# Performance work log

Measured on AMD Instinct MI355X. Metric: run time of the kernel, lower is better.

## Reference

```python
import jax, jax.numpy as jnp
import numpy as np

B = 32768
IN_DIM = 768
HIDDENS = [2048, 1024, 512]
EMBED_DIM = 128
NUM_EMB = 1024
DEPTH = 3


def setup_inputs() -> dict:
    key = jax.random.key(0)
    ks = jax.random.split(key, 20)
    d = {"x": jax.random.normal(ks[0], (B, IN_DIM), dtype=jnp.float32)}
    # Encoder: in -> h0 -> h1 -> h2 -> embed  (weights stored as [in, out])
    enc_dims = [IN_DIM] + HIDDENS + [EMBED_DIM]
    for i in range(4):
        fan_in = enc_dims[i]
        d[f"enc_W{i+1}"] = jax.random.normal(ks[1 + i], (enc_dims[i], enc_dims[i + 1]), dtype=jnp.float32) / np.sqrt(fan_in)
        d[f"enc_b{i+1}"] = jnp.zeros((enc_dims[i + 1],), dtype=jnp.float32)
    # Decoder: embed -> h0 -> h1 -> h2 -> in
    dec_dims = [EMBED_DIM] + HIDDENS + [IN_DIM]
    for i in range(4):
        fan_in = dec_dims[i]
        d[f"dec_W{i+1}"] = jax.random.normal(ks[5 + i], (dec_dims[i], dec_dims[i + 1]), dtype=jnp.float32) / np.sqrt(fan_in)
        d[f"dec_b{i+1}"] = jnp.zeros((dec_dims[i + 1],), dtype=jnp.float32)
    # Codebook (nn.Embedding weight, initialized ~ N(0,1) as in the module)
    d["codebook"] = jax.random.normal(ks[9], (NUM_EMB, EMBED_DIM), dtype=jnp.float32)
    return d


def _encoder(x, W1, b1, W2, b2, W3, b3, W4, b4):
    x = jax.nn.relu(x @ W1 + b1)
    x = jax.nn.relu(x @ W2 + b2)
    x = jax.nn.relu(x @ W3 + b3)
    return x @ W4 + b4


def _decoder(x, W1, b1, W2, b2, W3, b3, W4, b4):
    x = jax.nn.relu(x @ W1 + b1)
    x = jax.nn.relu(x @ W2 + b2)
    x = jax.nn.relu(x @ W3 + b3)
    return x @ W4 + b4


def reference(x,
              enc_W1, enc_b1, enc_W2, enc_b2, enc_W3, enc_b3, enc_W4, enc_b4,
              dec_W1, dec_b1, dec_W2, dec_b2, dec_W3, dec_b3, dec_W4, dec_b4,
              codebook):
    z = _encoder(x, enc_W1, enc_b1, enc_W2, enc_b2, enc_W3, enc_b3, enc_W4, enc_b4)
    z_det = jax.lax.stop_gradient(z)

    cb_sq = jnp.sum(codebook * codebook, axis=1)  # [K]
    residue = z_det
    z_hat = jnp.zeros_like(z_det)
    codes = []
    for _ in range(DEPTH):  # residual quantization loop
        # squared L2 distances [B, K]
        dist = (jnp.sum(residue * residue, axis=1, keepdims=True)
                + cb_sq
                - 2.0 * residue @ codebook.T)
        idx = jnp.argmin(dist, axis=1)          # [B]
        codes.append(idx)
        z_hat = z_hat + codebook[idx]           # gather codebook vectors
        residue = z_det - z_hat
    all_codes = jnp.stack(codes, axis=1)        # [B, DEPTH] int

    # straight-through estimator: forward uses z_hat, grad flows through z
    z_flow = z + jax.lax.stop_gradient(z_hat - z)
    x_recon = _decoder(z_flow, dec_W1, dec_b1, dec_W2, dec_b2, dec_W3, dec_b3, dec_W4, dec_b4)
    return (x_recon, all_codes)
```

## Files before the change

kernel.cpp:

```cpp
#include <hip/hip_runtime.h>

#define FLT_MAX_C 3.402823466e+38f

typedef __attribute__((ext_vector_type(8))) __bf16 bf16x8;
typedef __attribute__((ext_vector_type(4))) float f32x4;

static __device__ __forceinline__ ushort f2bf(float x) {
    union { float f; unsigned u; } v; v.f = x;
    unsigned r = (v.u + 0x7FFFu + ((v.u >> 16) & 1u)) >> 16;
    return (ushort)r;
}

template<bool RELU>
__device__ __forceinline__ void gemm_f32_dev(
    const float* __restrict__ A, const float* __restrict__ W,
    const float* __restrict__ bias, float* __restrict__ C, int K, int N)
{
    __shared__ float As[8][128];
    __shared__ float Bs[8][132];
    const int tid = threadIdx.x;
    const int bm = blockIdx.y << 7;
    const int bn = blockIdx.x << 7;

    const int la_row = tid >> 1;
    const int la_k   = (tid & 1) << 2;
    const int lb_row = tid >> 5;
    const int lb_col = (tid & 31) << 2;
    const int tm4 = (tid >> 4) << 2;
    const int tn4 = (tid & 15) << 2;

    float acc[8][8];
    #pragma unroll
    for (int i = 0; i < 8; ++i)
        #pragma unroll
        for (int j = 0; j < 8; ++j) acc[i][j] = 0.f;

    const float* aptr = A + (size_t)(bm + la_row) * K + la_k;
    const float* bptr = W + (size_t)lb_row * N + bn + lb_col;

    float4 av = *(const float4*)(aptr);
    float4 bv = *(const float4*)(bptr);

    for (int k0 = 0; k0 < K; k0 += 8) {
        __syncthreads();
        As[la_k + 0][la_row] = av.x;
        As[la_k + 1][la_row] = av.y;
        As[la_k + 2][la_row] = av.z;
        As[la_k + 3][la_row] = av.w;
        *(float4*)(&Bs[lb_row][lb_col]) = bv;
        __syncthreads();
        if (k0 + 8 < K) {
            av = *(const float4*)(aptr + k0 + 8);
            bv = *(const float4*)(bptr + (size_t)(k0 + 8) * N);
        }
        #pragma unroll
        for (int kk = 0; kk < 8; ++kk) {
            float a[8], b[8];
            *(float4*)(a)     = *(const float4*)(&As[kk][tm4]);
            *(float4*)(a + 4) = *(const float4*)(&As[kk][tm4 + 64]);
            *(float4*)(b)     = *(const float4*)(&Bs[kk][tn4]);
            *(float4*)(b + 4) = *(const float4*)(&Bs[kk][tn4 + 64]);
            #pragma unroll
            for (int i = 0; i < 8; ++i)
                #pragma unroll
                for (int j = 0; j < 8; ++j)
                    acc[i][j] = fmaf(a[i], b[j], acc[i][j]);
        }
    }

    float bv0[8];
    #pragma unroll
    for (int j = 0; j < 8; ++j)
        bv0[j] = bias[bn + tn4 + (j < 4 ? j : 60 + j)];

    #pragma unroll
    for (int i = 0; i < 8; ++i) {
        int row = bm + tm4 + (i < 4 ? i : 60 + i);
        float* cp = C + (size_t)row * N + bn + tn4;
        float4 v0, v1;
        v0.x = acc[i][0] + bv0[0]; v0.y = acc[i][1] + bv0[1];
        v0.z = acc[i][2] + bv0[2]; v0.w = acc[i][3] + bv0[3];
        v1.x = acc[i][4] + bv0[4]; v1.y = acc[i][5] + bv0[5];
        v1.z = acc[i][6] + bv0[6]; v1.w = acc[i][7] + bv0[7];
        if (RELU) {
            v0.x = fmaxf(v0.x, 0.f); v0.y = fmaxf(v0.y, 0.f);
            v0.z = fmaxf(v0.z, 0.f); v0.w = fmaxf(v0.w, 0.f);
            v1.x = fmaxf(v1.x, 0.f); v1.y = fmaxf(v1.y, 0.f);
            v1.z = fmaxf(v1.z, 0.f); v1.w = fmaxf(v1.w, 0.f);
        }
        *(float4*)(cp) = v0;
        *(float4*)(cp + 64) = v1;
    }
}

template<bool RELU>
__device__ __forceinline__ void gemm_f32_wide_dev(
    const float* __restrict__ A, const float* __restrict__ W,
    const float* __restrict__ bias, float* __restrict__ C, int K, int N)
{
    __shared__ float As[8][128];
    __shared__ float Bs[8][260];
    const int tid = threadIdx.x;
    const int bm = blockIdx.y << 7;
    const int bn = blockIdx.x << 8;

    const int la_row = tid >> 1;
    const int la_k   = (tid & 1) << 2;
    const int tm4 = (tid >> 4) << 2;
    const int tn4 = (tid & 15) << 2;
    const int bf_row  = tid >> 6;
    const int bf_col4 = (tid & 63) << 2;

    float acc[8][16];
    #pragma unroll
    for (int i = 0; i < 8; ++i)
        #pragma unroll
        for (int j = 0; j < 16; ++j) acc[i][j] = 0.f;

    const float* aptr = A + (size_t)(bm + la_row) * K + la_k;
    const float* bptr = W + (size_t)bf_row * N + bn + bf_col4;

    float4 av = *(const float4*)(aptr);
    float4 bv0 = *(const float4*)(bptr);
    float4 bv1 = *(const float4*)(bptr + (size_t)4 * N);

    for (int k0 = 0; k0 < K; k0 += 8) {
        __syncthreads();
        As[la_k + 0][la_row] = av.x;
        As[la_k + 1][la_row] = av.y;
        As[la_k + 2][la_row] = av.z;
        As[la_k + 3][la_row] = av.w;
        *(float4*)(&Bs[bf_row][bf_col4])     = bv0;
        *(float4*)(&Bs[bf_row + 4][bf_col4]) = bv1;
        __syncthreads();
        if (k0 + 8 < K) {
            av  = *(const float4*)(aptr + k0 + 8);
            bv0 = *(const float4*)(bptr + (size_t)(k0 + 8) * N);
            bv1 = *(const float4*)(bptr + (size_t)(k0 + 12) * N);
        }
        #pragma unroll
        for (int kk = 0; kk < 8; ++kk) {
            float a[8], b[16];
            *(float4*)(a)      = *(const float4*)(&As[kk][tm4]);
            *(float4*)(a + 4)  = *(const float4*)(&As[kk][tm4 + 64]);
            #pragma unroll
            for (int q = 0; q < 4; ++q)
                *(float4*)(b + q * 4) = *(const float4*)(&Bs[kk][tn4 + 64 * q]);
            #pragma unroll
            for (int i = 0; i < 8; ++i)
                #pragma unroll
                for (int j = 0; j < 16; ++j)
                    acc[i][j] = fmaf(a[i], b[j], acc[i][j]);
        }
    }

    float bb[16];
    #pragma unroll
    for (int q = 0; q < 4; ++q)
        #pragma unroll
        for (int jj = 0; jj < 4; ++jj)
            bb[q * 4 + jj] = bias[bn + tn4 + 64 * q + jj];

    #pragma unroll
    for (int i = 0; i < 8; ++i) {
        int row = bm + tm4 + (i < 4 ? i : 60 + i);
        float* cp = C + (size_t)row * N + bn + tn4;
        #pragma unroll
        for (int q = 0; q < 4; ++q) {
            float4 v;
            v.x = acc[i][q * 4 + 0] + bb[q * 4 + 0];
            v.y = acc[i][q * 4 + 1] + bb[q * 4 + 1];
            v.z = acc[i][q * 4 + 2] + bb[q * 4 + 2];
            v.w = acc[i][q * 4 + 3] + bb[q * 4 + 3];
            if (RELU) {
                v.x = fmaxf(v.x, 0.f); v.y = fmaxf(v.y, 0.f);
                v.z = fmaxf(v.z, 0.f); v.w = fmaxf(v.w, 0.f);
            }
            *(float4*)(cp + 64 * q) = v;
        }
    }
}

template<bool RELU>
__device__ __forceinline__ void gemm_f32_64_dev(
    const float* __restrict__ A, const float* __restrict__ W,
    const float* __restrict__ bias, float* __restrict__ C, int K, int N)
{
    __shared__ float As[16][64];
    __shared__ float Bs[16][132];
    const int tid = threadIdx.x;
    const int bm = blockIdx.y << 6;
    const int bn = blockIdx.x << 7;

    const int la_row = tid & 63;
    const int la_k   = (tid >> 6) << 2;
    const int lb_row = tid >> 5;
    const int lb_col = (tid & 31) << 2;
    const int tr = tid >> 4;
    const int tc = tid & 15;

    float acc[4][8];
    #pragma unroll
    for (int i = 0; i < 4; ++i)
        #pragma unroll
        for (int j = 0; j < 8; ++j) acc[i][j] = 0.f;

    const float* aptr = A + (size_t)(bm + la_row) * K + la_k;
    const float* bptr = W + (size_t)lb_row * N + bn + lb_col;

    float4 av = *(const float4*)(aptr);
    float4 bv0 = *(const float4*)(bptr);
    float4 bv1 = *(const float4*)(bptr + (size_t)8 * N);

    for (int k0 = 0; k0 < K; k0 += 16) {
        __syncthreads();
        As[la_k + 0][la_row] = av.x;
        As[la_k + 1][la_row] = av.y;
        As[la_k + 2][la_row] = av.z;
        As[la_k + 3][la_row] = av.w;
        *(float4*)(&Bs[lb_row][lb_col]) = bv0;
        *(float4*)(&Bs[lb_row + 8][lb_col]) = bv1;
        __syncthreads();
        if (k0 + 16 < K) {
            av  = *(const float4*)(aptr + k0 + 16);
            bv0 = *(const float4*)(bptr + (size_t)(k0 + 16) * N);
            bv1 = *(const float4*)(bptr + (size_t)(k0 + 24) * N);
        }
        #pragma unroll
        for (int kk = 0; kk < 16; ++kk) {
            float a[4], b[8];
            *(float4*)(a) = *(const float4*)(&As[kk][tr << 2]);
            *(float4*)(b)     = *(const float4*)(&Bs[kk][tc << 2]);
            *(float4*)(b + 4) = *(const float4*)(&Bs[kk][(tc << 2) + 64]);
            #pragma unroll
            for (int i = 0; i < 4; ++i)
                #pragma unroll
                for (int j = 0; j < 8; ++j)
                    acc[i][j] = fmaf(a[i], b[j], acc[i][j]);
        }
    }

    float bb[8];
    #pragma unroll
    for (int j = 0; j < 8; ++j)
        bb[j] = bias[bn + (tc << 2) + (j < 4 ? j : 60 + j)];

    #pragma unroll
    for (int i = 0; i < 4; ++i) {
        float* cp = C + (size_t)(bm + (tr << 2) + i) * N + bn + (tc << 2);
        float4 v0, v1;
        v0.x = acc[i][0] + bb[0]; v0.y = acc[i][1] + bb[1];
        v0.z = acc[i][2] + bb[2]; v0.w = acc[i][3] + bb[3];
        v1.x = acc[i][4] + bb[4]; v1.y = acc[i][5] + bb[5];
        v1.z = acc[i][6] + bb[6]; v1.w = acc[i][7] + bb[7];
        if (RELU) {
            v0.x = fmaxf(v0.x, 0.f); v0.y = fmaxf(v0.y, 0.f);
            v0.z = fmaxf(v0.z, 0.f); v0.w = fmaxf(v0.w, 0.f);
            v1.x = fmaxf(v1.x, 0.f); v1.y = fmaxf(v1.y, 0.f);
            v1.z = fmaxf(v1.z, 0.f); v1.w = fmaxf(v1.w, 0.f);
        }
        *(float4*)(cp) = v0;
        *(float4*)(cp + 64) = v1;
    }
}

template<bool RELU, bool OUTF32>
__device__ __forceinline__ void gemm_bf16_dev(
    const ushort* __restrict__ A, const ushort* __restrict__ Wt,
    const float* __restrict__ bias, void* __restrict__ C, int K, int N)
{
    __shared__ __align__(16) ushort As[128][64];
    __shared__ __align__(16) ushort Bs[128][64];
    const int tid  = threadIdx.x;
    const int lane = tid & 63;
    const int wv   = tid >> 6;
    const int wm   = (wv >> 1) << 6;
    const int wn   = (wv & 1) << 6;
    const int bm   = blockIdx.y << 7;
    const int bn   = blockIdx.x << 7;
    const int lr   = lane & 15;
    const int lh   = lane >> 4;

    f32x4 acc[4][4];
    #pragma unroll
    for (int m = 0; m < 4; ++m)
        #pragma unroll
        for (int n = 0; n < 4; ++n) acc[m][n] = (f32x4){0.f, 0.f, 0.f, 0.f};

    for (int k0 = 0; k0 < K; k0 += 64) {
        __syncthreads();
        #pragma unroll
        for (int i = 0; i < 4; ++i) {
            const int c    = wv * 4 + i;
            const int boff = c * 1024 + lane * 16;
            const int r    = boff >> 7;
            const int cbt  = boff & 127;
            const char* sa = (const char*)A  + (((size_t)(bm + r) * K + k0) << 1) + cbt;
            const char* sb = (const char*)Wt + (((size_t)(bn + r) * K + k0) << 1) + cbt;
            __builtin_amdgcn_global_load_lds((const void*)sa, (void*)(&As[0][0] + c * 512), 16, 0, 0);
            __builtin_amdgcn_global_load_lds((const void*)sb, (void*)(&Bs[0][0] + c * 512), 16, 0, 0);
        }
        __syncthreads();
        #pragma unroll
        for (int kk = 0; kk < 64; kk += 32) {
            bf16x8 af[4], bfr[4];
            #pragma unroll
            for (int m = 0; m < 4; ++m)
                af[m] = *(const bf16x8*)&As[wm + m * 16 + lr][kk + lh * 8];
            #pragma unroll
            for (int n = 0; n < 4; ++n)
                bfr[n] = *(const bf16x8*)&Bs[wn + n * 16 + lr][kk + lh * 8];
            #pragma unroll
            for (int m = 0; m < 4; ++m)
                #pragma unroll
                for (int n = 0; n < 4; ++n)
                    acc[m][n] = __builtin_amdgcn_mfma_f32_16x16x32_bf16(
                        af[m], bfr[n], acc[m][n], 0, 0, 0);
        }
    }

    #pragma unroll
    for (int n = 0; n < 4; ++n) {
        const int col = bn + wn + n * 16 + lr;
        const float bcol = bias[col];
        #pragma unroll
        for (int m = 0; m < 4; ++m) {
            #pragma unroll
            for (int i = 0; i < 4; ++i) {
                const int row = bm + wm + m * 16 + lh * 4 + i;
                float v = acc[m][n][i] + bcol;
                if (RELU) v = fmaxf(v, 0.f);
                if (OUTF32) ((float*)C)[(size_t)row * N + col] = v;
                else        ((ushort*)C)[(size_t)row * N + col] = f2bf(v);
            }
        }
    }
}

__global__ __launch_bounds__(256) void enc1_gemm(const float* A, const float* W, const float* b, float* C)
{ gemm_f32_wide_dev<true>(A, W, b, C, 768, 2048); }
__global__ __launch_bounds__(256) void enc2_gemm(const float* A, const float* W, const float* b, float* C)
{ gemm_f32_wide_dev<true>(A, W, b, C, 2048, 1024); }
__global__ __launch_bounds__(256) void enc3_gemm(const float* A, const float* W, const float* b, float* C)
{ gemm_f32_dev<true>(A, W, b, C, 1024, 512); }
__global__ __launch_bounds__(256) void enc4_gemm(const float* A, const float* W, const float* b, float* C)
{ gemm_f32_64_dev<false>(A, W, b, C, 512, 128); }
__global__ __launch_bounds__(256) void dec1_gemm(const ushort* A, const ushort* Wt, const float* b, void* C)
{ gemm_bf16_dev<true, false>(A, Wt, b, C, 128, 2048); }
__global__ __launch_bounds__(256) void dec2_gemm(const ushort* A, const ushort* Wt, const float* b, void* C)
{ gemm_bf16_dev<true, false>(A, Wt, b, C, 2048, 1024); }
__global__ __launch_bounds__(256) void dec3_gemm(const ushort* A, const ushort* Wt, const float* b, void* C)
{ gemm_bf16_dev<true, false>(A, Wt, b, C, 1024, 512); }
__global__ __launch_bounds__(256) void dec4_gemm(const ushort* A, const ushort* Wt, const float* b, void* C)
{ gemm_bf16_dev<false, true>(A, Wt, b, C, 512, 768); }

__device__ __forceinline__ void wt_convert_dev(
    const float* __restrict__ W, ushort* __restrict__ Wt, int K, int N,
    int bx, int by, void* smem)
{
    ushort (*t)[65] = (ushort(*)[65])smem;
    const int kb = by << 6, nb = bx << 6;
    const int c  = threadIdx.x & 63;
    const int r0 = (threadIdx.x >> 6) << 4;
    #pragma unroll
    for (int i = 0; i < 16; ++i)
        t[r0 + i][c] = f2bf(W[(size_t)(kb + r0 + i) * N + nb + c]);
    __syncthreads();
    #pragma unroll
    for (int i = 0; i < 16; ++i)
        Wt[(size_t)(nb + r0 + i) * K + kb + c] = t[c][r0 + i];
}

__global__ __launch_bounds__(256) void prep_all(
    const float* dW1, const float* dW2, const float* dW3, const float* dW4,
    ushort* Wt1, ushort* Wt2, ushort* Wt3, ushort* Wt4,
    const float* cb, float* sq, float* cbt)
{
    __shared__ float smem[64][65];
    int b = blockIdx.x;
    if (b < 64)  { wt_convert_dev(dW1, Wt1, 128,  2048, b % 32, b / 32, smem); return; }
    b -= 64;
    if (b < 512) { wt_convert_dev(dW2, Wt2, 2048, 1024, b % 16, b / 16, smem); return; }
    b -= 512;
    if (b < 128) { wt_convert_dev(dW3, Wt3, 1024, 512,  b % 8,  b / 8,  smem); return; }
    b -= 128;
    if (b < 96)  { wt_convert_dev(dW4, Wt4, 512,  768,  b % 12, b / 12, smem); return; }
    b -= 96;
    if (b < 4) {
        int k = b * 256 + threadIdx.x;
        const float* r = cb + ((size_t)k << 7);
        float s = 0.f;
        #pragma unroll 8
        for (int d = 0; d < 128; ++d) s = fmaf(r[d], r[d], s);
        sq[k] = s;
        return;
    }
    b -= 4;
    {
        const int kb = (b % 16) << 6;
        const int db = (b / 16) << 6;
        const int c  = threadIdx.x & 63;
        const int r0 = (threadIdx.x >> 6) << 4;
        #pragma unroll
        for (int i = 0; i < 16; ++i)
            smem[r0 + i][c] = cb[(size_t)(kb + r0 + i) * 128 + db + c];
        __syncthreads();
        #pragma unroll
        for (int i = 0; i < 16; ++i)
            cbt[(size_t)(db + r0 + i) * 1024 + kb + c] = smem[c][r0 + i];
    }
}

__global__ __launch_bounds__(256) void rq_all(
    const float* __restrict__ z, const float* __restrict__ cbt,
    const float* __restrict__ sq, const float* __restrict__ cb,
    ushort* __restrict__ ZHb, float* __restrict__ codes)
{
    __shared__ float As[128][68];
    __shared__ float Bs[32][132];
    __shared__ float sqs[1024];
    __shared__ float rrs[64];

    const int tid = threadIdx.x;
    const int bm  = blockIdx.x << 6;
    const int tr  = tid >> 4;
    const int c   = tid & 15;
    const int tn4 = c << 2;
    const int lb_row = tid >> 5;
    const int lb_col = (tid & 31) << 2;

    #pragma unroll
    for (int i = 0; i < 4; ++i) sqs[tid + (i << 8)] = sq[tid + (i << 8)];

    float zh[4][8];
    #pragma unroll
    for (int i = 0; i < 4; ++i) {
        const int r_  = (tr << 2) + i;
        const float* zp = z + (size_t)(bm + r_) * 128 + (c << 3);
        float4 z0 = *(const float4*)(zp);
        float4 z1 = *(const float4*)(zp + 4);
        #pragma unroll
        for (int j = 0; j < 8; ++j) zh[i][j] = 0.f;
        As[(c << 3) + 0][r_] = z0.x; As[(c << 3) + 1][r_] = z0.y;
        As[(c << 3) + 2][r_] = z0.z; As[(c << 3) + 3][r_] = z0.w;
        As[(c << 3) + 4][r_] = z1.x; As[(c << 3) + 5][r_] = z1.y;
        As[(c << 3) + 6][r_] = z1.z; As[(c << 3) + 7][r_] = z1.w;
        float p = z0.x * z0.x;
        p = fmaf(z0.y, z0.y, p); p = fmaf(z0.z, z0.z, p);
        p = fmaf(z0.w, z0.w, p); p = fmaf(z1.x, z1.x, p);
        p = fmaf(z1.y, z1.y, p); p = fmaf(z1.z, z1.z, p);
        p = fmaf(z1.w, z1.w, p);
        #pragma unroll
        for (int o = 8; o >= 1; o >>= 1) p += __shfl_xor(p, o);
        if (c == 0) rrs[r_] = p;
    }
    __syncthreads();

    for (int t = 0; t < 3; ++t) {
        float rr_[4];
        #pragma unroll
        for (int i = 0; i < 4; ++i) rr_[i] = rrs[(tr << 2) + i];

        float best_d[4] = {FLT_MAX_C, FLT_MAX_C, FLT_MAX_C, FLT_MAX_C};
        int   best_i[4] = {0, 0, 0, 0};

        for (int bx = 0; bx < 8; ++bx) {
            const int bn = bx << 7;
            const float* bptr = cbt + (size_t)lb_row * 1024 + bn + lb_col;
            float4 bv0 = *(const float4*)(bptr);
            float4 bv1 = *(const float4*)(bptr + (size_t)8  * 1024);
            float4 bv2 = *(const float4*)(bptr + (size_t)16 * 1024);
            float4 bv3 = *(const float4*)(bptr + (size_t)24 * 1024);

            float acc[4][8];
            #pragma unroll
            for (int i = 0; i < 4; ++i)
                #pragma unroll
                for (int j = 0; j < 8; ++j) acc[i][j] = 0.f;

            for (int k0 = 0; k0 < 128; k0 += 32) {
                __syncthreads();
                *(float4*)(&Bs[lb_row +  0][lb_col]) = bv0;
                *(float4*)(&Bs[lb_row +  8][lb_col]) = bv1;
                *(float4*)(&Bs[lb_row + 16][lb_col]) = bv2;
                *(float4*)(&Bs[lb_row + 24][lb_col]) = bv3;
                __syncthreads();
                if (k0 + 32 < 128) {
                    bv0 = *(const float4*)(bptr + (size_t)(k0 + 32) * 1024);
                    bv1 = *(const float4*)(bptr + (size_t)(k0 + 40) * 1024);
                    bv2 = *(const float4*)(bptr + (size_t)(k0 + 48) * 1024);
                    bv3 = *(const float4*)(bptr + (size_t)(k0 + 56) * 1024);
                }
                #pragma unroll
                for (int kk = 0; kk < 32; ++kk) {
                    float a[4], b[8];
                    *(float4*)(a)     = *(const float4*)(&As[k0 + kk][tr << 2]);
                    *(float4*)(b)     = *(const float4*)(&Bs[kk][tn4]);
                    *(float4*)(b + 4) = *(const float4*)(&Bs[kk][tn4 + 64]);
                    #pragma unroll
                    for (int i = 0; i < 4; ++i)
                        #pragma unroll
                        for (int j = 0; j < 8; ++j)
                            acc[i][j] = fmaf(a[i], b[j], acc[i][j]);
                }
            }
            #pragma unroll
            for (int i = 0; i < 4; ++i) {
                #pragma unroll
                for (int j = 0; j < 8; ++j) {
                    const int col = bn + tn4 + (j < 4 ? j : 60 + j);
                    float d = (rr_[i] + sqs[col]) - 2.f * acc[i][j];
                    if (d < best_d[i]) { best_d[i] = d; best_i[i] = col; }
                }
            }
        }

        #pragma unroll
        for (int i = 0; i < 4; ++i) {
            float bd = best_d[i]; int bi = best_i[i];
            #pragma unroll
            for (int o = 8; o >= 1; o >>= 1) {
                float od = __shfl_xor(bd, o);
                int   oi = __shfl_xor(bi, o);
                if (od < bd || (od == bd && oi < bi)) { bd = od; bi = oi; }
            }
            best_i[i] = bi;
        }

        __syncthreads();

        #pragma unroll
        for (int i = 0; i < 4; ++i) {
            const int r_  = (tr << 2) + i;
            const int row = bm + r_;
            if (c == 0) codes[(size_t)row * 3 + t] = (float)best_i[i];

            const float* cbp = cb + ((size_t)best_i[i] << 7) + (c << 3);
            float4 c0 = *(const float4*)(cbp);
            float4 c1 = *(const float4*)(cbp + 4);
            zh[i][0] += c0.x; zh[i][1] += c0.y;
            zh[i][2] += c0.z; zh[i][3] += c0.w;
            zh[i][4] += c1.x; zh[i][5] += c1.y;
            zh[i][6] += c1.z; zh[i][7] += c1.w;

            if (t < 2) {
                const float* zp = z + (size_t)row * 128 + (c << 3);
                float4 z0 = *(const float4*)(zp);
                float4 z1 = *(const float4*)(zp + 4);
                float r0 = z0.x - zh[i][0], r1 = z0.y - zh[i][1];
                float r2 = z0.z - zh[i][2], r3 = z0.w - zh[i][3];
                float r4 = z1.x - zh[i][4], r5 = z1.y - zh[i][5];
                float r6 = z1.z - zh[i][6], r7 = z1.w - zh[i][7];
                As[(c << 3) + 0][r_] = r0; As[(c << 3) + 1][r_] = r1;
                As[(c << 3) + 2][r_] = r2; As[(c << 3) + 3][r_] = r3;
                As[(c << 3) + 4][r_] = r4; As[(c << 3) + 5][r_] = r5;
                As[(c << 3) + 6][r_] = r6; As[(c << 3) + 7][r_] = r7;
                float p = r0 * r0;
                p = fmaf(r1, r1, p); p = fmaf(r2, r2, p);
                p = fmaf(r3, r3, p); p = fmaf(r4, r4, p);
                p = fmaf(r5, r5, p); p = fmaf(r6, r6, p);
                p = fmaf(r7, r7, p);
                #pragma unroll
                for (int o = 8; o >= 1; o >>= 1) p += __shfl_xor(p, o);
                if (c == 0) rrs[r_] = p;
            } else {
                ushort4 o0, o1;
                o0.x = f2bf(zh[i][0]); o0.y = f2bf(zh[i][1]);
                o0.z = f2bf(zh[i][2]); o0.w = f2bf(zh[i][3]);
                o1.x = f2bf(zh[i][4]); o1.y = f2bf(zh[i][5]);
                o1.z = f2bf(zh[i][6]); o1.w = f2bf(zh[i][7]);
                ushort* zbp = ZHb + (size_t)row * 128 + (c << 3);
                *(ushort4*)(zbp)     = o0;
                *(ushort4*)(zbp + 4) = o1;
            }
        }
        if (t < 2) __syncthreads();
    }
}

extern "C" void kernel_launch(void* const* d_in, const int* in_sizes, int n_in,
                              void* d_out, int out_size, void* d_ws, size_t ws_size,
                              hipStream_t stream)
{
    const float* x   = (const float*)d_in[0];
    const float* eW1 = (const float*)d_in[1];
    const float* eb1 = (const float*)d_in[2];
    const float* eW2 = (const float*)d_in[3];
    const float* eb2 = (const float*)d_in[4];
    const float* eW3 = (const float*)d_in[5];
    const float* eb3 = (const float*)d_in[6];
    const float* eW4 = (const float*)d_in[7];
    const float* eb4 = (const float*)d_in[8];
    const float* dW1 = (const float*)d_in[9];
    const float* db1 = (const float*)d_in[10];
    const float* dW2 = (const float*)d_in[11];
    const float* db2 = (const float*)d_in[12];
    const float* dW3 = (const float*)d_in[13];
    const float* db3 = (const float*)d_in[14];
    const float* dW4 = (const float*)d_in[15];
    const float* db4 = (const float*)d_in[16];
    const float* cb  = (const float*)d_in[17];

    float* out   = (float*)d_out;
    float* codes = out + (size_t)32768 * 768;

    ushort* Wt1 = (ushort*)d_ws;
    ushort* Wt2 = Wt1 + (size_t)2048 * 128;
    ushort* Wt3 = Wt2 + (size_t)1024 * 2048;
    ushort* Wt4 = Wt3 + (size_t)512 * 1024;
    float*  sq  = (float*)(Wt4 + (size_t)768 * 512);
    float*  cbt = sq + 1024;
    float*  act = cbt + (size_t)128 * 1024;
    const size_t fixed_b = (char*)act - (char*)d_ws;

    int mc = 32768;
    while (mc > 1024) {
        if (fixed_b + (size_t)mc * 15104 <= ws_size) break;
        mc >>= 1;
    }

    float*  R1  = act;
    float*  R2  = R1 + (size_t)mc * 2048;
    float*  R3  = R2 + (size_t)mc * 1024;
    float*  RZ  = R3 + (size_t)mc * 512;
    ushort* ZHb = (ushort*)(RZ + (size_t)mc * 128);
    ushort* D1  = (ushort*)R1;
    ushort* D2  = (ushort*)R2;
    ushort* D3  = (ushort*)R3;

    prep_all<<<836, 256, 0, stream>>>(dW1, dW2, dW3, dW4, Wt1, Wt2, Wt3, Wt4,
                                      cb, sq, cbt);

    const int mg = mc >> 7;
    for (int r0 = 0; r0 < 32768; r0 += mc) {
        const float* xi     = x     + (size_t)r0 * 768;
        float*       outi   = out   + (size_t)r0 * 768;
        float*       codesi = codes + (size_t)r0 * 3;
        enc1_gemm<<<dim3( 8, mg), 256, 0, stream>>>(xi, eW1, eb1, R1);
        enc2_gemm<<<dim3( 4, mg), 256, 0, stream>>>(R1, eW2, eb2, R2);
        enc3_gemm<<<dim3( 4, mg), 256, 0, stream>>>(R2, eW3, eb3, R3);
        enc4_gemm<<<dim3( 1, mc >> 6), 256, 0, stream>>>(R3, eW4, eb4, RZ);
        rq_all<<<mc >> 6, 256, 0, stream>>>(RZ, cbt, sq, cb, ZHb, codesi);
        dec1_gemm<<<dim3(16, mg), 256, 0, stream>>>(ZHb, Wt1, db1, D1);
        dec2_gemm<<<dim3( 8, mg), 256, 0, stream>>>(D1,  Wt2, db2, D2);
        dec3_gemm<<<dim3( 4, mg), 256, 0, stream>>>(D2,  Wt3, db3, D3);
        dec4_gemm<<<dim3( 6, mg), 256, 0, stream>>>(D3,  Wt4, db4, outi);
    }
}
```

Before: 3.778 ms.

## Merge weight prep into enc1 launch and add XCD-aware block swizzle to GEMMs

```diff
diff --git a/kernel.cpp b/kernel.cpp
--- a/kernel.cpp
+++ b/kernel.cpp
@@ -11,16 +11,28 @@
     return (ushort)r;
 }
 
+static __device__ __forceinline__ void xcd_swz(int& bx, int& by) {
+    const int gx = gridDim.x;
+    const int nwg = gx * gridDim.y;
+    const int bid = blockIdx.y * gx + blockIdx.x;
+    const int q = nwg >> 3, r = nwg & 7;
+    const int xcd = bid & 7, lid = bid >> 3;
+    const int swz = (xcd < r ? xcd * (q + 1) : r * (q + 1) + (xcd - r) * q) + lid;
+    bx = swz % gx;
+    by = swz / gx;
+}
+
 template<bool RELU>
 __device__ __forceinline__ void gemm_f32_dev(
     const float* __restrict__ A, const float* __restrict__ W,
-    const float* __restrict__ bias, float* __restrict__ C, int K, int N)
+    const float* __restrict__ bias, float* __restrict__ C, int K, int N,
+    int bxi, int byi)
 {
     __shared__ float As[8][128];
     __shared__ float Bs[8][132];
     const int tid = threadIdx.x;
-    const int bm = blockIdx.y << 7;
-    const int bn = blockIdx.x << 7;
+    const int bm = byi << 7;
+    const int bn = bxi << 7;
 
     const int la_row = tid >> 1;
     const int la_k   = (tid & 1) << 2;
@@ -96,13 +108,14 @@
 template<bool RELU>
 __device__ __forceinline__ void gemm_f32_wide_dev(
     const float* __restrict__ A, const float* __restrict__ W,
-    const float* __restrict__ bias, float* __restrict__ C, int K, int N)
-{
-    __shared__ float As[8][128];
-    __shared__ float Bs[8][260];
+    const float* __restrict__ bias, float* __restrict__ C, int K, int N,
+    int bxi, int byi, void* smem)
+{
+    float (*As)[128] = (float(*)[128])smem;
+    float (*Bs)[260] = (float(*)[260])((char*)smem + 4096);
     const int tid = threadIdx.x;
-    const int bm = blockIdx.y << 7;
-    const int bn = blockIdx.x << 8;
+    const int bm = byi << 7;
+    const int bn = bxi << 8;
 
     const int la_row = tid >> 1;
     const int la_k   = (tid & 1) << 2;
@@ -184,13 +197,14 @@
 template<bool RELU>
 __device__ __forceinline__ void gemm_f32_64_dev(
     const float* __restrict__ A, const float* __restrict__ W,
-    const float* __restrict__ bias, float* __restrict__ C, int K, int N)
+    const float* __restrict__ bias, float* __restrict__ C, int K, int N,
+    int bxi, int byi)
 {
     __shared__ float As[16][64];
     __shared__ float Bs[16][132];
     const int tid = threadIdx.x;
-    const int bm = blockIdx.y << 6;
-    const int bn = blockIdx.x << 7;
+    const int bm = byi << 6;
+    const int bn = bxi << 7;
 
     const int la_row = tid & 63;
     const int la_k   = (tid >> 6) << 2;
@@ -267,7 +281,8 @@
 template<bool RELU, bool OUTF32>
 __device__ __forceinline__ void gemm_bf16_dev(
     const ushort* __restrict__ A, const ushort* __restrict__ Wt,
-    const float* __restrict__ bias, void* __restrict__ C, int K, int N)
+    const float* __restrict__ bias, void* __restrict__ C, int K, int N,
+    int bxi, int byi)
 {
     __shared__ __align__(16) ushort As[128][64];
     __shared__ __align__(16) ushort Bs[128][64];
@@ -276,8 +291,8 @@
     const int wv   = tid >> 6;
     const int wm   = (wv >> 1) << 6;
     const int wn   = (wv & 1) << 6;
-    const int bm   = blockIdx.y << 7;
-    const int bn   = blockIdx.x << 7;
+    const int bm   = byi << 7;
+    const int bn   = bxi << 7;
     const int lr   = lane & 15;
     const int lh   = lane >> 4;
 
@@ -337,23 +352,6 @@
     }
 }
 
-__global__ __launch_bounds__(256) void enc1_gemm(const float* A, const float* W, const float* b, float* C)
-{ gemm_f32_wide_dev<true>(A, W, b, C, 768, 2048); }
-__global__ __launch_bounds__(256) void enc2_gemm(const float* A, const float* W, const float* b, float* C)
-{ gemm_f32_wide_dev<true>(A, W, b, C, 2048, 1024); }
-__global__ __launch_bounds__(256) void enc3_gemm(const float* A, const float* W, const float* b, float* C)
-{ gemm_f32_dev<true>(A, W, b, C, 1024, 512); }
-__global__ __launch_bounds__(256) void enc4_gemm(const float* A, const float* W, const float* b, float* C)
-{ gemm_f32_64_dev<false>(A, W, b, C, 512, 128); }
-__global__ __launch_bounds__(256) void dec1_gemm(const ushort* A, const ushort* Wt, const float* b, void* C)
-{ gemm_bf16_dev<true, false>(A, Wt, b, C, 128, 2048); }
-__global__ __launch_bounds__(256) void dec2_gemm(const ushort* A, const ushort* Wt, const float* b, void* C)
-{ gemm_bf16_dev<true, false>(A, Wt, b, C, 2048, 1024); }
-__global__ __launch_bounds__(256) void dec3_gemm(const ushort* A, const ushort* Wt, const float* b, void* C)
-{ gemm_bf16_dev<true, false>(A, Wt, b, C, 1024, 512); }
-__global__ __launch_bounds__(256) void dec4_gemm(const ushort* A, const ushort* Wt, const float* b, void* C)
-{ gemm_bf16_dev<false, true>(A, Wt, b, C, 512, 768); }
-
 __device__ __forceinline__ void wt_convert_dev(
     const float* __restrict__ W, ushort* __restrict__ Wt, int K, int N,
     int bx, int by, void* smem)
@@ -371,13 +369,12 @@
         Wt[(size_t)(nb + r0 + i) * K + kb + c] = t[c][r0 + i];
 }
 
-__global__ __launch_bounds__(256) void prep_all(
+__device__ __forceinline__ void prep_dispatch(
+    int b,
     const float* dW1, const float* dW2, const float* dW3, const float* dW4,
     ushort* Wt1, ushort* Wt2, ushort* Wt3, ushort* Wt4,
-    const float* cb, float* sq, float* cbt)
-{
-    __shared__ float smem[64][65];
-    int b = blockIdx.x;
+    const float* cb, float* sq, float* cbt, void* smem)
+{
     if (b < 64)  { wt_convert_dev(dW1, Wt1, 128,  2048, b % 32, b / 32, smem); return; }
     b -= 64;
     if (b < 512) { wt_convert_dev(dW2, Wt2, 2048, 1024, b % 16, b / 16, smem); return; }
@@ -397,19 +394,53 @@
     }
     b -= 4;
     {
+        float (*t)[65] = (float(*)[65])smem;
         const int kb = (b % 16) << 6;
         const int db = (b / 16) << 6;
         const int c  = threadIdx.x & 63;
         const int r0 = (threadIdx.x >> 6) << 4;
         #pragma unroll
         for (int i = 0; i < 16; ++i)
-            smem[r0 + i][c] = cb[(size_t)(kb + r0 + i) * 128 + db + c];
+            t[r0 + i][c] = cb[(size_t)(kb + r0 + i) * 128 + db + c];
         __syncthreads();
         #pragma unroll
         for (int i = 0; i < 16; ++i)
-            cbt[(size_t)(db + r0 + i) * 1024 + kb + c] = smem[c][r0 + i];
-    }
-}
+            cbt[(size_t)(db + r0 + i) * 1024 + kb + c] = t[c][r0 + i];
+    }
+}
+
+__global__ __launch_bounds__(256) void enc1_prep(
+    const float* A, const float* W, const float* b, float* C, int encb,
+    const float* dW1, const float* dW2, const float* dW3, const float* dW4,
+    ushort* Wt1, ushort* Wt2, ushort* Wt3, ushort* Wt4,
+    const float* cb, float* sq, float* cbt)
+{
+    __shared__ __align__(16) char pool[16640];
+    const int bid = blockIdx.x;
+    if (bid < encb) {
+        gemm_f32_wide_dev<true>(A, W, b, C, 768, 2048, bid & 7, bid >> 3, pool);
+    } else {
+        prep_dispatch(bid - encb, dW1, dW2, dW3, dW4, Wt1, Wt2, Wt3, Wt4,
+                      cb, sq, cbt, pool);
+    }
+}
+
+__global__ __launch_bounds__(256) void enc2_gemm(const float* A, const float* W, const float* b, float* C)
+{ __shared__ __align__(16) char pool[12416];
+  int bx, by; xcd_swz(bx, by);
+  gemm_f32_wide_dev<true>(A, W, b, C, 2048, 1024, bx, by, pool); }
+__global__ __launch_bounds__(256) void enc3_gemm(const float* A, const float* W, const float* b, float* C)
+{ int bx, by; xcd_swz(bx, by); gemm_f32_dev<true>(A, W, b, C, 1024, 512, bx, by); }
+__global__ __launch_bounds__(256) void enc4_gemm(const float* A, const float* W, const float* b, float* C)
+{ int bx, by; xcd_swz(bx, by); gemm_f32_64_dev<false>(A, W, b, C, 512, 128, bx, by); }
+__global__ __launch_bounds__(256) void dec1_gemm(const ushort* A, const ushort* Wt, const float* b, void* C)
+{ int bx, by; xcd_swz(bx, by); gemm_bf16_dev<true, false>(A, Wt, b, C, 128, 2048, bx, by); }
+__global__ __launch_bounds__(256) void dec2_gemm(const ushort* A, const ushort* Wt, const float* b, void* C)
+{ int bx, by; xcd_swz(bx, by); gemm_bf16_dev<true, false>(A, Wt, b, C, 2048, 1024, bx, by); }
+__global__ __launch_bounds__(256) void dec3_gemm(const ushort* A, const ushort* Wt, const float* b, void* C)
+{ int bx, by; xcd_swz(bx, by); gemm_bf16_dev<true, false>(A, Wt, b, C, 1024, 512, bx, by); }
+__global__ __launch_bounds__(256) void dec4_gemm(const ushort* A, const ushort* Wt, const float* b, void* C)
+{ int bx, by; xcd_swz(bx, by); gemm_bf16_dev<false, true>(A, Wt, b, C, 512, 768, bx, by); }
 
 __global__ __launch_bounds__(256) void rq_all(
     const float* __restrict__ z, const float* __restrict__ cbt,
@@ -628,15 +659,18 @@
     ushort* D2  = (ushort*)R2;
     ushort* D3  = (ushort*)R3;
 
-    prep_all<<<836, 256, 0, stream>>>(dW1, dW2, dW3, dW4, Wt1, Wt2, Wt3, Wt4,
-                                      cb, sq, cbt);
-
     const int mg = mc >> 7;
+    bool first = true;
     for (int r0 = 0; r0 < 32768; r0 += mc) {
         const float* xi     = x     + (size_t)r0 * 768;
         float*       outi   = out   + (size_t)r0 * 768;
         float*       codesi = codes + (size_t)r0 * 3;
-        enc1_gemm<<<dim3( 8, mg), 256, 0, stream>>>(xi, eW1, eb1, R1);
+        const int encb = 8 * mg;
+        const int prepb = first ? 836 : 0;
+        enc1_prep<<<encb + prepb, 256, 0, stream>>>(
+            xi, eW1, eb1, R1, encb,
+            dW1, dW2, dW3, dW4, Wt1, Wt2, Wt3, Wt4, cb, sq, cbt);
+        first = false;
         enc2_gemm<<<dim3( 4, mg), 256, 0, stream>>>(R1, eW2, eb2, R2);
         enc3_gemm<<<dim3( 4, mg), 256, 0, stream>>>(R2, eW3, eb3, R3);
         enc4_gemm<<<dim3( 1, mc >> 6), 256, 0, stream>>>(R3, eW4, eb4, RZ);
```

After: 3.779 ms. No clear change (+0.0%).
